# Optimization experiments

Measured on AMD Instinct MI355X. Metric: run time of the kernel, lower is better.

## Reference

```python
import jax, jax.numpy as jnp
import numpy as np
import math

F = 64        # num_features (multiplicity of each irrep)
N = 16000     # nodes
E = 256000    # edges (avg_num_neighbors = 16)
S = 4         # num_species
DE = 32       # scalar edge feature dim (radial basis)
W = 128       # interaction_mlp_width
AVG_NEIGH = 16.0
SQ2 = math.sqrt(2.0)
SQ3 = math.sqrt(3.0)


def setup_inputs() -> dict:
    key = jax.random.key(0)
    ks = jax.random.split(key, 32)
    def nrm(k, shape, scale=1.0):
        return jax.random.normal(k, shape, dtype=jnp.float32) * scale
    inp = {}
    # forward args
    inp["vectors"] = nrm(ks[0], (E, 1, 3))
    inp["lengths"] = jax.random.uniform(ks[1], (E, 1), dtype=jnp.float32)
    inp["node_s"] = nrm(ks[2], (N, F))            # 64x0e part of node_feats
    inp["node_v"] = nrm(ks[3], (N, F, 3))         # 64x1o part of node_feats
    inp["scalar_edge_feats"] = nrm(ks[4], (E, DE))
    inp["node_specie"] = jax.random.randint(ks[5], (N,), 0, S)
    inp["senders"] = jax.random.randint(ks[6], (E,), 0, N)
    inp["receivers"] = jax.random.randint(ks[7], (E,), 0, N)
    # parameters (e3nn Linear = per-irrep channel mixing, fan-in normalized; bias only on 0e)
    inp["W_up_s"] = nrm(ks[8], (F, F), F ** -0.5); inp["b_up_s"] = jnp.zeros((F,), jnp.float32)
    inp["W_up_v"] = nrm(ks[9], (F, F), F ** -0.5)
    din = 2 * F + DE + 1
    inp["mlp_W1"] = nrm(ks[10], (din, W), din ** -0.5); inp["mlp_b1"] = jnp.zeros((W,), jnp.float32)
    inp["mlp_W2"] = nrm(ks[11], (W, W), W ** -0.5); inp["mlp_b2"] = jnp.zeros((W,), jnp.float32)
    inp["mlp_W3"] = nrm(ks[12], (W, 3 * F), W ** -0.5); inp["mlp_b3"] = jnp.zeros((3 * F,), jnp.float32)
    inp["W_dn_s"] = nrm(ks[13], (F, F), F ** -0.5); inp["b_dn_s"] = jnp.zeros((F,), jnp.float32)
    inp["W_dn_v"] = nrm(ks[14], (2 * F, F), (2 * F) ** -0.5)
    # symmetric contraction weights (per species, per channel); correlation=2
    inp["w_sc_s"] = nrm(ks[15], (S, 3, F), 3 ** -0.5)   # paths to 0e: x0, x0^2, (x1.x1)/sqrt3
    inp["w_sc_v"] = nrm(ks[16], (S, 2, F), 2 ** -0.5)   # paths to 1o: x1, x0*x1
    inp["W_pb_s"] = nrm(ks[17], (F, F), F ** -0.5); inp["b_pb_s"] = jnp.zeros((F,), jnp.float32)
    inp["W_pb_v"] = nrm(ks[18], (F, F), F ** -0.5)
    inp["W_r1_s"] = nrm(ks[19], (F, 2 * F), F ** -0.5); inp["b_r1_s"] = jnp.zeros((2 * F,), jnp.float32)
    inp["W_r1_v"] = nrm(ks[20], (F, F), F ** -0.5)
    inp["W_r2_s"] = nrm(ks[21], (F, 1), F ** -0.5); inp["b_r2"] = jnp.zeros((1,), jnp.float32)
    inp["W_r2_v"] = nrm(ks[22], (F, 1), F ** -0.5)
    return inp


def reference(vectors, lengths, node_s, node_v, scalar_edge_feats, node_specie,
              senders, receivers,
              W_up_s, b_up_s, W_up_v,
              mlp_W1, mlp_b1, mlp_W2, mlp_b2, mlp_W3, mlp_b3,
              W_dn_s, b_dn_s, W_dn_v,
              w_sc_s, w_sc_v, W_pb_s, b_pb_s, W_pb_v,
              W_r1_s, b_r1_s, W_r1_v, W_r2_s, b_r2, W_r2_v):
    n = node_s.shape[0]
    # --- spherical harmonics, sh_irreps='1o', component normalization, normalize=False ---
    edge_v = SQ3 * vectors[:, 0, :]                              # [E,3]

    # --- InteractionBlock: linear_up ---
    h_s = node_s @ W_up_s + b_up_s                               # [N,F]
    h_v = jnp.einsum('nfi,fg->ngi', node_v, W_up_v)              # [N,F,3]

    # --- MessagePassingConvolution ---
    m_s = h_s[senders]                                           # [E,F] 0e
    m_v = h_v[senders]                                           # [E,F,3] 1o
    # tensor product with edge 1o, filtered to 0e+1o (unitary CG):
    tp_s = jnp.einsum('efi,ei->ef', m_v, edge_v) / SQ3           # 1o x 1o -> 0e  [E,F]
    tp_v1 = m_s[:, :, None] * edge_v[:, None, :]                 # 0e x 1o -> 1o  [E,F,3]
    tp_v2 = jnp.cross(m_v, edge_v[:, None, :]) / SQ2             # 1o x 1o -> 1o  [E,F,3]
    # scalar MLP mix (one scalar weight per output irrep = 3F)
    mlp_in = jnp.concatenate([m_s, h_s[receivers], scalar_edge_feats, lengths], axis=1)
    h = jax.nn.silu(mlp_in @ mlp_W1 + mlp_b1)
    h = jax.nn.silu(h @ mlp_W2 + mlp_b2)
    mix = h @ mlp_W3 + mlp_b3                                    # [E,3F]
    mix_s, mix_v1, mix_v2 = mix[:, :F], mix[:, F:2 * F], mix[:, 2 * F:]
    tp_s = tp_s * mix_s
    tp_v = jnp.concatenate([tp_v1 * mix_v1[:, :, None], tp_v2 * mix_v2[:, :, None]], axis=1)  # [E,2F,3]
    # scatter-add to receivers, normalize by avg_num_neighbors
    agg_s = jax.ops.segment_sum(tp_s, receivers, num_segments=n) / AVG_NEIGH   # [N,F]
    agg_v = jax.ops.segment_sum(tp_v, receivers, num_segments=n) / AVG_NEIGH   # [N,2F,3]
    # linear_down
    f_s = agg_s @ W_dn_s + b_dn_s                                # [N,F]
    f_v = jnp.einsum('nfi,fg->ngi', agg_v, W_dn_v)               # [N,F,3]

    # --- EquivariantProductBasisBlock: symmetric contraction (correlation=2), per-species ---
    ws = w_sc_s[node_specie]                                     # [N,3,F]
    wv = w_sc_v[node_specie]                                     # [N,2,F]
    vv = jnp.sum(f_v * f_v, axis=-1) / SQ3                       # 1o (x) 1o -> 0e, symmetric
    sc_s = ws[:, 0] * f_s + ws[:, 1] * (f_s * f_s) + ws[:, 2] * vv           # [N,F]
    sc_v = wv[:, 0][:, :, None] * f_v + wv[:, 1][:, :, None] * (f_s[:, :, None] * f_v)  # [N,F,3]
    p_s = sc_s @ W_pb_s + b_pb_s                                 # node_feats 0e out
    p_v = jnp.einsum('nfi,fg->ngi', sc_v, W_pb_v)                # node_feats 1o out

    # --- NonLinearReadoutBlock: linear to (2F x 0e + F x 1o), gate, linear to 1x0e+1x1o ---
    r_s = p_s @ W_r1_s + b_r1_s                                  # [N,2F]
    r_v = jnp.einsum('nfi,fg->ngi', p_v, W_r1_v)                 # [N,F,3]
    act = jax.nn.silu(r_s[:, :F])
    gates = jax.nn.silu(r_s[:, F:])
    g_v = gates[:, :, None] * r_v                                # gated vectors
    out_s = act @ W_r2_s + b_r2                                  # [N,1]  0e output
    out_v = jnp.einsum('nfi,fo->noi', g_v, W_r2_v)               # [N,1,3] 1o output
    return out_s, out_v, p_s, p_v
```

## Files before the change

kernel.cpp:

```cpp
#include <hip/hip_runtime.h>

typedef short bf16x8 __attribute__((ext_vector_type(8)));
typedef float f32x4  __attribute__((ext_vector_type(4)));
typedef unsigned short ushort_t;
typedef _Float16 half_t;

__device__ __forceinline__ float silu(float x) {
    float t = __expf(-x);
    return x * __builtin_amdgcn_rcpf(1.f + t);
}

__device__ __forceinline__ ushort_t f2bs(float x) {
    union { float f; unsigned int u; } v; v.f = x;
    unsigned int r = v.u + 0x7FFF + ((v.u >> 16) & 1);
    return (ushort_t)(r >> 16);
}
__device__ __forceinline__ ushort_t f2bs_t(float x) {
    union { float f; unsigned int u; } v; v.f = x;
    return (ushort_t)(v.u >> 16);
}
__device__ __forceinline__ float bs2f(ushort_t x) {
    union { unsigned int u; float f; } v; v.u = ((unsigned int)x) << 16; return v.f;
}

constexpr int N_   = 16000;
constexpr int E_   = 256000;
constexpr int Fd   = 64;

constexpr float SQ3f    = 1.7320508075688772f;
constexpr float INV_SQ3 = 0.5773502691896258f;
constexpr float INV_SQ2 = 0.7071067811865476f;
constexpr float INV_AVG = 0.0625f;

constexpr int OFF_OS = 0;
constexpr int OFF_OV = N_;
constexpr int OFF_PS = OFF_OV + 3 * N_;
constexpr int OFF_PV = OFF_PS + N_ * Fd;

constexpr int W1P_SZ = 6 * 8 * 512;
constexpr int W2P_SZ = 4 * 8 * 512;
constexpr int W3P_SZ = 4 * 12 * 512;

constexpr int CTR_W = 320;

__global__ __launch_bounds__(256) void pack_kernel(
    const float* __restrict__ W1, const float* __restrict__ W2,
    const float* __restrict__ W3,
    ushort_t* __restrict__ W1p, ushort_t* __restrict__ W2p,
    ushort_t* __restrict__ W3p)
{
    int idx = blockIdx.x * 256 + threadIdx.x;
    if (idx < W1P_SZ) {
        int j = idx & 7, lane = (idx >> 3) & 63, tile = idx >> 9;
        int c = tile >> 3, t = tile & 7;
        int k = c * 32 + (lane >> 4) * 8 + j;
        int n = t * 16 + (lane & 15);
        W1p[idx] = f2bs(k < 161 ? W1[k * 128 + n] : 0.f);
    } else if (idx < W1P_SZ + W2P_SZ) {
        int q = idx - W1P_SZ;
        int j = q & 7, lane = (q >> 3) & 63, tile = q >> 9;
        int c = tile >> 3, t = tile & 7;
        int k = c * 32 + (lane >> 4) * 8 + j;
        int n = t * 16 + (lane & 15);
        W2p[q] = f2bs(W2[k * 128 + n]);
    } else {
        int q = idx - W1P_SZ - W2P_SZ;
        int j = q & 7, lane = (q >> 3) & 63, tile = q >> 9;
        int c = tile / 12, t = tile % 12;
        int k = c * 32 + (lane >> 4) * 8 + j;
        int n = t * 16 + (lane & 15);
        W3p[q] = f2bs(W3[k * 192 + n]);
    }
}

__global__ __launch_bounds__(64, 4) void up_kernel(
    const float* __restrict__ node_s, const float* __restrict__ node_v,
    const float* __restrict__ W_up_s, const float* __restrict__ b_up_s,
    const float* __restrict__ W_up_v,
    const int* __restrict__ receivers, int* __restrict__ cnt,
    ushort_t* __restrict__ hs_bf, float* __restrict__ h_v)
{
    __shared__ float ns[4][64];
    __shared__ float nv[4][64][3];
    const int n0 = blockIdx.x * 4;
    const int g  = threadIdx.x;

    {
        int e = blockIdx.x * 64 + g;
        atomicAdd(&cnt[receivers[e]], 1);
    }

    #pragma unroll
    for (int j = 0; j < 4; j++) ns[j][g] = node_s[(n0 + j) * 64 + g];
    for (int idx = g; idx < 4 * 192; idx += 64) {
        int j = idx / 192, r = idx - j * 192;
        nv[j][r / 3][r % 3] = node_v[(size_t)n0 * 192 + idx];
    }
    __syncthreads();

    float as[4], a0[4], a1[4], a2[4];
    float bb = b_up_s[g];
    #pragma unroll
    for (int j = 0; j < 4; j++) { as[j] = bb; a0[j] = a1[j] = a2[j] = 0.f; }
    #pragma unroll 4
    for (int f = 0; f < 64; f++) {
        float wss = W_up_s[f * 64 + g];
        float wv  = W_up_v[f * 64 + g];
        #pragma unroll
        for (int j = 0; j < 4; j++) {
            as[j] += ns[j][f] * wss;
            a0[j] += nv[j][f][0] * wv;
            a1[j] += nv[j][f][1] * wv;
            a2[j] += nv[j][f][2] * wv;
        }
    }
    #pragma unroll
    for (int j = 0; j < 4; j++) {
        hs_bf[(n0 + j) * 64 + g] = f2bs(as[j]);
        h_v[(n0 + j) * 192 + 0 * 64 + g] = a0[j];
        h_v[(n0 + j) * 192 + 1 * 64 + g] = a1[j];
        h_v[(n0 + j) * 192 + 2 * 64 + g] = a2[j];
    }
}

__global__ __launch_bounds__(1024) void scan_kernel(
    const int* __restrict__ cnt, int* __restrict__ base, int* __restrict__ cursor)
{
    __shared__ int part[1024];
    const int t = threadIdx.x;
    int v[16];
    int s = 0;
    if (t < 1000) {
        const int4* c4 = (const int4*)(cnt + t * 16);
        #pragma unroll
        for (int q = 0; q < 4; q++) {
            int4 w = c4[q];
            v[q * 4 + 0] = w.x; v[q * 4 + 1] = w.y;
            v[q * 4 + 2] = w.z; v[q * 4 + 3] = w.w;
            s += w.x + w.y + w.z + w.w;
        }
    }
    part[t] = s;
    __syncthreads();
    for (int off = 1; off < 1024; off <<= 1) {
        int u = (t >= off) ? part[t - off] : 0;
        __syncthreads();
        part[t] += u;
        __syncthreads();
    }
    if (t < 1000) {
        int run = part[t] - s;
        int b[16];
        #pragma unroll
        for (int i = 0; i < 16; i++) { b[i] = run; run += v[i]; }
        int4* bb = (int4*)(base + t * 16);
        int4* cc = (int4*)(cursor + t * 16);
        #pragma unroll
        for (int q = 0; q < 4; q++) {
            int4 w = { b[q * 4], b[q * 4 + 1], b[q * 4 + 2], b[q * 4 + 3] };
            bb[q] = w;
            cc[q] = w;
        }
    }
}

__global__ __launch_bounds__(256, 3) void edge_mlp_kernel(
    const float* __restrict__ lengths, const float* __restrict__ sef,
    const int* __restrict__ senders, const int* __restrict__ receivers,
    const float* __restrict__ vectors,
    const float* __restrict__ b1f, const float* __restrict__ b2f,
    const float* __restrict__ b3f,
    const ushort_t* __restrict__ hs_bf, const float* __restrict__ h_v,
    const ushort_t* __restrict__ W1p, const ushort_t* __restrict__ W2p,
    const ushort_t* __restrict__ W3p,
    int* __restrict__ cursor, float4* __restrict__ evx,
    half_t* __restrict__ ctr)
{
    __shared__ ushort_t Als[64 * 200];
    __shared__ ushort_t Hs[64 * 136];
    __shared__ int perm_s[64];
    __shared__ int snd_s[64];
    __shared__ float ev_s[64][3];

    const int tid  = threadIdx.x;
    const int wave = tid >> 6, lane = tid & 63;
    const int quad = lane >> 4, l4 = lane & 15;
    const int e0   = blockIdx.x * 64;

    if (tid < 64) {
        int e = e0 + tid;
        int p = atomicAdd(&cursor[receivers[e]], 1);
        perm_s[tid] = p;
        snd_s[tid] = senders[e];
        float v0 = SQ3f * vectors[e * 3 + 0];
        float v1 = SQ3f * vectors[e * 3 + 1];
        float v2 = SQ3f * vectors[e * 3 + 2];
        ev_s[tid][0] = v0; ev_s[tid][1] = v1; ev_s[tid][2] = v2;
        float4 mt; mt.x = v0; mt.y = v1; mt.z = v2; mt.w = 0.f;
        evx[p] = mt;
    }

    {
        const int e  = tid & 63;
        const int ge = e0 + e;
        const int snd = senders[ge];
        const int rcv = receivers[ge];
        for (int c = tid >> 6; c < 24; c += 4) {
            bf16x8 v;
            if (c < 8) {
                v = *(const bf16x8*)(hs_bf + snd * 64 + c * 8);
            } else if (c < 16) {
                v = *(const bf16x8*)(hs_bf + rcv * 64 + (c - 8) * 8);
            } else if (c < 20) {
                const float4 s0 = *(const float4*)(sef + (size_t)ge * 32 + (c - 16) * 8);
                const float4 s1 = *(const float4*)(sef + (size_t)ge * 32 + (c - 16) * 8 + 4);
                v[0] = (short)f2bs(s0.x); v[1] = (short)f2bs(s0.y);
                v[2] = (short)f2bs(s0.z); v[3] = (short)f2bs(s0.w);
                v[4] = (short)f2bs(s1.x); v[5] = (short)f2bs(s1.y);
                v[6] = (short)f2bs(s1.z); v[7] = (short)f2bs(s1.w);
            } else if (c == 20) {
                v = (bf16x8){0,0,0,0,0,0,0,0};
                v[0] = (short)f2bs(lengths[ge]);
            } else {
                v = (bf16x8){0,0,0,0,0,0,0,0};
            }
            *(bf16x8*)(&Als[e * 200 + c * 8]) = v;
        }
    }
    __syncthreads();

    const bf16x8* B1 = (const bf16x8*)W1p;
    const bf16x8* B2 = (const bf16x8*)W2p;
    const bf16x8* B3 = (const bf16x8*)W3p;

    {
        f32x4 acc[2][4];
        #pragma unroll
        for (int ti = 0; ti < 2; ti++)
            #pragma unroll
            for (int m = 0; m < 4; m++) acc[ti][m] = (f32x4){0,0,0,0};
        #pragma unroll
        for (int c = 0; c < 6; c++) {
            bf16x8 b0 = B1[(c * 8 + wave * 2 + 0) * 64 + lane];
            bf16x8 b1 = B1[(c * 8 + wave * 2 + 1) * 64 + lane];
            #pragma unroll
            for (int m = 0; m < 4; m++) {
                bf16x8 a = *(const bf16x8*)(&Als[(m * 16 + l4) * 200 + c * 32 + quad * 8]);
                acc[0][m] = __builtin_amdgcn_mfma_f32_16x16x32_bf16(a, b0, acc[0][m], 0, 0, 0);
                acc[1][m] = __builtin_amdgcn_mfma_f32_16x16x32_bf16(a, b1, acc[1][m], 0, 0, 0);
            }
        }
        #pragma unroll
        for (int ti = 0; ti < 2; ti++) {
            int t = wave * 2 + ti;
            float bb = b1f[t * 16 + l4];
            #pragma unroll
            for (int m = 0; m < 4; m++)
                #pragma unroll
                for (int r = 0; r < 4; r++)
                    Hs[(m * 16 + quad * 4 + r) * 136 + t * 16 + l4] =
                        f2bs_t(silu(acc[ti][m][r] + bb));
        }
    }
    __syncthreads();

    {
        f32x4 acc[2][4];
        #pragma unroll
        for (int ti = 0; ti < 2; ti++)
            #pragma unroll
            for (int m = 0; m < 4; m++) acc[ti][m] = (f32x4){0,0,0,0};
        #pragma unroll
        for (int c = 0; c < 4; c++) {
            bf16x8 b0 = B2[(c * 8 + wave * 2 + 0) * 64 + lane];
            bf16x8 b1 = B2[(c * 8 + wave * 2 + 1) * 64 + lane];
            #pragma unroll
            for (int m = 0; m < 4; m++) {
                bf16x8 a = *(const bf16x8*)(&Hs[(m * 16 + l4) * 136 + c * 32 + quad * 8]);
                acc[0][m] = __builtin_amdgcn_mfma_f32_16x16x32_bf16(a, b0, acc[0][m], 0, 0, 0);
                acc[1][m] = __builtin_amdgcn_mfma_f32_16x16x32_bf16(a, b1, acc[1][m], 0, 0, 0);
            }
        }
        #pragma unroll
        for (int ti = 0; ti < 2; ti++) {
            int t = wave * 2 + ti;
            float bb = b2f[t * 16 + l4];
            #pragma unroll
            for (int m = 0; m < 4; m++)
                #pragma unroll
                for (int r = 0; r < 4; r++)
                    Als[(m * 16 + quad * 4 + r) * 136 + t * 16 + l4] =
                        f2bs_t(silu(acc[ti][m][r] + bb));
        }
    }
    __syncthreads();

    {
        f32x4 acc[3][4];
        #pragma unroll
        for (int ti = 0; ti < 3; ti++)
            #pragma unroll
            for (int m = 0; m < 4; m++) acc[ti][m] = (f32x4){0,0,0,0};
        #pragma unroll
        for (int c = 0; c < 4; c++) {
            bf16x8 b0 = B3[(c * 12 + wave * 3 + 0) * 64 + lane];
            bf16x8 b1 = B3[(c * 12 + wave * 3 + 1) * 64 + lane];
            bf16x8 b2 = B3[(c * 12 + wave * 3 + 2) * 64 + lane];
            #pragma unroll
            for (int m = 0; m < 4; m++) {
                bf16x8 a = *(const bf16x8*)(&Als[(m * 16 + l4) * 136 + c * 32 + quad * 8]);
                acc[0][m] = __builtin_amdgcn_mfma_f32_16x16x32_bf16(a, b0, acc[0][m], 0, 0, 0);
                acc[1][m] = __builtin_amdgcn_mfma_f32_16x16x32_bf16(a, b1, acc[1][m], 0, 0, 0);
                acc[2][m] = __builtin_amdgcn_mfma_f32_16x16x32_bf16(a, b2, acc[2][m], 0, 0, 0);
            }
        }
        __syncthreads();
        #pragma unroll
        for (int ti = 0; ti < 3; ti++) {
            int t = wave * 3 + ti;
            float bb = b3f[t * 16 + l4];
            #pragma unroll
            for (int m = 0; m < 4; m++)
                #pragma unroll
                for (int r = 0; r < 4; r++)
                    Als[(m * 16 + quad * 4 + r) * 200 + t * 16 + l4] =
                        f2bs(acc[ti][m][r] + bb);
        }
    }
    __syncthreads();

    {
        const int g = lane;
        #pragma unroll 4
        for (int j = 0; j < 16; j++) {
            const int el = wave * 16 + j;
            const int se = snd_s[el];
            const int p  = perm_s[el];
            const float ev0 = ev_s[el][0], ev1 = ev_s[el][1], ev2 = ev_s[el][2];
            const float m0 = h_v[(size_t)se * 192 + 0 * 64 + g];
            const float m1 = h_v[(size_t)se * 192 + 1 * 64 + g];
            const float m2 = h_v[(size_t)se * 192 + 2 * 64 + g];
            const float ms = bs2f(hs_bf[se * 64 + g]);
            const float mixs  = bs2f(Als[el * 200 +   0 + g]);
            const float mixv1 = bs2f(Als[el * 200 +  64 + g]);
            const float mixv2 = bs2f(Als[el * 200 + 128 + g]);
            half_t* row = ctr + (size_t)p * CTR_W;
            row[  0 + g] = (half_t)((m0 * ev0 + m1 * ev1 + m2 * ev2) * mixs);
            row[ 64 + g] = (half_t)(ms * mixv1);
            row[128 + g] = (half_t)((m1 * ev2 - m2 * ev1) * mixv2);
            row[192 + g] = (half_t)((m2 * ev0 - m0 * ev2) * mixv2);
            row[256 + g] = (half_t)((m0 * ev1 - m1 * ev0) * mixv2);
        }
    }
}

__global__ __launch_bounds__(256, 2) void node_fused_kernel(
    const int* __restrict__ base, const int* __restrict__ cnt,
    const float4* __restrict__ evx,
    const half_t* __restrict__ ctr,
    const int* __restrict__ specie,
    const float* __restrict__ W_dn_s, const float* __restrict__ b_dn_s,
    const float* __restrict__ W_dn_v,
    const float* __restrict__ w_sc_s, const float* __restrict__ w_sc_v,
    const float* __restrict__ W_pb_s, const float* __restrict__ b_pb_s,
    const float* __restrict__ W_pb_v,
    const float* __restrict__ W_r1_s, const float* __restrict__ b_r1_s,
    const float* __restrict__ W_r1_v,
    const float* __restrict__ W_r2_s, const float* __restrict__ b_r2,
    const float* __restrict__ W_r2_v,
    float* __restrict__ out)
{
    __shared__ float as_l[4][64];
    __shared__ float av_l[4][128][3];
    __shared__ float scs[4][64];
    __shared__ float scv[4][64][3];
    __shared__ float ps_[4][64];
    __shared__ float pv_[4][64][3];
    __shared__ float4 lmeta[4][64];

    const int tid = threadIdx.x;
    const int w   = tid >> 6;
    const int g   = tid & 63;
    const int n   = blockIdx.x * 4 + w;

    const int b = base[n];
    const int c = cnt[n];
    float accSa = 0.f, accSb = 0.f;
    float a10a = 0.f, a11a = 0.f, a12a = 0.f;
    float a20a = 0.f, a21a = 0.f, a22a = 0.f;
    float a10b = 0.f, a11b = 0.f, a12b = 0.f;
    float a20b = 0.f, a21b = 0.f, a22b = 0.f;

    for (int done = 0; done < c; done += 64) {
        int m = min(64, c - done);
        if (g < m) lmeta[w][g] = evx[b + done + g];
        int i = 0;
        for (; i + 1 < m; i += 2) {
            const float4 t1 = lmeta[w][i];
            const float4 t2 = lmeta[w][i + 1];
            const half_t* r1 = ctr + (size_t)(b + done + i) * CTR_W;
            const half_t* r2 = r1 + CTR_W;
            const float cs1 = (float)r1[g];
            const float k1  = (float)r1[64 + g];
            const float c10 = (float)r1[128 + g];
            const float c11 = (float)r1[192 + g];
            const float c12 = (float)r1[256 + g];
            const float cs2 = (float)r2[g];
            const float k2  = (float)r2[64 + g];
            const float c20 = (float)r2[128 + g];
            const float c21 = (float)r2[192 + g];
            const float c22 = (float)r2[256 + g];

            accSa += cs1; accSb += cs2;
            a10a += k1 * t1.x; a11a += k1 * t1.y; a12a += k1 * t1.z;
            a10b += k2 * t2.x; a11b += k2 * t2.y; a12b += k2 * t2.z;
            a20a += c10; a21a += c11; a22a += c12;
            a20b += c20; a21b += c21; a22b += c22;
        }
        if (i < m) {
            const float4 t1 = lmeta[w][i];
            const half_t* r1 = ctr + (size_t)(b + done + i) * CTR_W;
            const float cs1 = (float)r1[g];
            const float k1  = (float)r1[64 + g];
            accSa += cs1;
            a10a += k1 * t1.x; a11a += k1 * t1.y; a12a += k1 * t1.z;
            a20a += (float)r1[128 + g];
            a21a += (float)r1[192 + g];
            a22a += (float)r1[256 + g];
        }
    }
    as_l[w][g] = (accSa + accSb) * (INV_SQ3 * INV_AVG);
    av_l[w][g][0] = (a10a + a10b) * INV_AVG;
    av_l[w][g][1] = (a11a + a11b) * INV_AVG;
    av_l[w][g][2] = (a12a + a12b) * INV_AVG;
    av_l[w][64 + g][0] = (a20a + a20b) * (INV_SQ2 * INV_AVG);
    av_l[w][64 + g][1] = (a21a + a21b) * (INV_SQ2 * INV_AVG);
    av_l[w][64 + g][2] = (a22a + a22b) * (INV_SQ2 * INV_AVG);

    float f_s = b_dn_s[g];
    #pragma unroll 8
    for (int f = 0; f < 64; f++) f_s += as_l[w][f] * W_dn_s[f * 64 + g];
    float fv0 = 0.f, fv1 = 0.f, fv2 = 0.f;
    #pragma unroll 8
    for (int f = 0; f < 128; f++) {
        float wt = W_dn_v[f * 64 + g];
        fv0 += av_l[w][f][0] * wt;
        fv1 += av_l[w][f][1] * wt;
        fv2 += av_l[w][f][2] * wt;
    }

    float vv = (fv0 * fv0 + fv1 * fv1 + fv2 * fv2) * INV_SQ3;
    int sp = specie[n];
    float ws0 = w_sc_s[sp * 192 + 0 * 64 + g];
    float ws1 = w_sc_s[sp * 192 + 1 * 64 + g];
    float ws2 = w_sc_s[sp * 192 + 2 * 64 + g];
    float wv0 = w_sc_v[sp * 128 + 0 * 64 + g];
    float wv1 = w_sc_v[sp * 128 + 1 * 64 + g];
    float sc_s = ws0 * f_s + ws1 * f_s * f_s + ws2 * vv;
    float kv = wv0 + wv1 * f_s;
    scs[w][g] = sc_s;
    scv[w][g][0] = kv * fv0;
    scv[w][g][1] = kv * fv1;
    scv[w][g][2] = kv * fv2;

    float p_s = b_pb_s[g];
    float pv0 = 0.f, pv1 = 0.f, pv2 = 0.f;
    #pragma unroll 8
    for (int f = 0; f < 64; f++) {
        float wps = W_pb_s[f * 64 + g];
        p_s += scs[w][f] * wps;
        float wpv = W_pb_v[f * 64 + g];
        pv0 += scv[w][f][0] * wpv;
        pv1 += scv[w][f][1] * wpv;
        pv2 += scv[w][f][2] * wpv;
    }
    ps_[w][g] = p_s;
    pv_[w][g][0] = pv0; pv_[w][g][1] = pv1; pv_[w][g][2] = pv2;

    out[OFF_PS + n * 64 + g] = p_s;
    out[OFF_PV + (size_t)n * 192 + g * 3 + 0] = pv0;
    out[OFF_PV + (size_t)n * 192 + g * 3 + 1] = pv1;
    out[OFF_PV + (size_t)n * 192 + g * 3 + 2] = pv2;

    float r0 = b_r1_s[g];
    float r1 = b_r1_s[g + 64];
    float rv0 = 0.f, rv1 = 0.f, rv2 = 0.f;
    #pragma unroll 8
    for (int f = 0; f < 64; f++) {
        float p = ps_[w][f];
        r0 += p * W_r1_s[f * 128 + g];
        r1 += p * W_r1_s[f * 128 + g + 64];
        float wrv = W_r1_v[f * 64 + g];
        rv0 += pv_[w][f][0] * wrv;
        rv1 += pv_[w][f][1] * wrv;
        rv2 += pv_[w][f][2] * wrv;
    }
    float act  = silu(r0);
    float gate = silu(r1);
    float o_s = act * W_r2_s[g];
    float wr2v = W_r2_v[g];
    float ov0 = gate * rv0 * wr2v;
    float ov1 = gate * rv1 * wr2v;
    float ov2 = gate * rv2 * wr2v;

    #pragma unroll
    for (int off = 32; off > 0; off >>= 1) {
        o_s += __shfl_down(o_s, off);
        ov0 += __shfl_down(ov0, off);
        ov1 += __shfl_down(ov1, off);
        ov2 += __shfl_down(ov2, off);
    }
    if (g == 0) {
        out[OFF_OS + n] = o_s + b_r2[0];
        out[OFF_OV + n * 3 + 0] = ov0;
        out[OFF_OV + n * 3 + 1] = ov1;
        out[OFF_OV + n * 3 + 2] = ov2;
    }
}

extern "C" void kernel_launch(void* const* d_in, const int* in_sizes, int n_in,
                              void* d_out, int out_size, void* d_ws, size_t ws_size,
                              hipStream_t stream)
{
    const float* vectors  = (const float*)d_in[0];
    const float* lengths  = (const float*)d_in[1];
    const float* node_s   = (const float*)d_in[2];
    const float* node_v   = (const float*)d_in[3];
    const float* sef      = (const float*)d_in[4];
    const int*  specie    = (const int*)d_in[5];
    const int*  senders   = (const int*)d_in[6];
    const int*  receivers = (const int*)d_in[7];
    const float* W_up_s   = (const float*)d_in[8];
    const float* b_up_s   = (const float*)d_in[9];
    const float* W_up_v   = (const float*)d_in[10];
    const float* mlp_W1   = (const float*)d_in[11];
    const float* mlp_b1   = (const float*)d_in[12];
    const float* mlp_W2   = (const float*)d_in[13];
    const float* mlp_b2   = (const float*)d_in[14];
    const float* mlp_W3   = (const float*)d_in[15];
    const float* mlp_b3   = (const float*)d_in[16];
    const float* W_dn_s   = (const float*)d_in[17];
    const float* b_dn_s   = (const float*)d_in[18];
    const float* W_dn_v   = (const float*)d_in[19];
    const float* w_sc_s   = (const float*)d_in[20];
    const float* w_sc_v   = (const float*)d_in[21];
    const float* W_pb_s   = (const float*)d_in[22];
    const float* b_pb_s   = (const float*)d_in[23];
    const float* W_pb_v   = (const float*)d_in[24];
    const float* W_r1_s   = (const float*)d_in[25];
    const float* b_r1_s   = (const float*)d_in[26];
    const float* W_r1_v   = (const float*)d_in[27];
    const float* W_r2_s   = (const float*)d_in[28];
    const float* b_r2     = (const float*)d_in[29];
    const float* W_r2_v   = (const float*)d_in[30];

    float* h_v = (float*)d_ws;
    half_t* ctr = (half_t*)(h_v + (size_t)N_ * 192);
    ushort_t* hs_bf = (ushort_t*)(ctr + (size_t)E_ * CTR_W);
    ushort_t* W1p   = hs_bf + (size_t)N_ * 64;
    ushort_t* W2p   = W1p + W1P_SZ;
    ushort_t* W3p   = W2p + W2P_SZ;
    float4* evx     = (float4*)((((size_t)(W3p + W3P_SZ)) + 15) & ~(size_t)15);
    int* cnt        = (int*)(evx + E_);
    int* base       = cnt + N_;
    int* cursor     = base + N_;

    float* out = (float*)d_out;

    hipMemsetAsync(cnt, 0, N_ * sizeof(int), stream);

    up_kernel<<<N_ / 4, 64, 0, stream>>>(node_s, node_v, W_up_s, b_up_s, W_up_v,
                                         receivers, cnt, hs_bf, h_v);
    pack_kernel<<<256, 256, 0, stream>>>(mlp_W1, mlp_W2, mlp_W3, W1p, W2p, W3p);
    scan_kernel<<<1, 1024, 0, stream>>>(cnt, base, cursor);

    edge_mlp_kernel<<<E_ / 64, 256, 0, stream>>>(
        lengths, sef, senders, receivers, vectors,
        mlp_b1, mlp_b2, mlp_b3,
        hs_bf, h_v, W1p, W2p, W3p, cursor, evx, ctr);

    node_fused_kernel<<<N_ / 4, 256, 0, stream>>>(
        base, cnt, evx,
        ctr, specie,
        W_dn_s, b_dn_s, W_dn_v, w_sc_s, w_sc_v,
        W_pb_s, b_pb_s, W_pb_v, W_r1_s, b_r1_s, W_r1_v,
        W_r2_s, b_r2, W_r2_v, out);
}
```

Before: 389.0 us.

## Process edges in receiver-sorted order and segment-reduce with atomics instead of staging

```diff
diff --git a/kernel.cpp b/kernel.cpp
--- a/kernel.cpp
+++ b/kernel.cpp
@@ -3,7 +3,6 @@
 typedef short bf16x8 __attribute__((ext_vector_type(8)));
 typedef float f32x4  __attribute__((ext_vector_type(4)));
 typedef unsigned short ushort_t;
-typedef _Float16 half_t;
 
 __device__ __forceinline__ float silu(float x) {
     float t = __expf(-x);
@@ -41,7 +40,7 @@
 constexpr int W2P_SZ = 4 * 8 * 512;
 constexpr int W3P_SZ = 4 * 12 * 512;
 
-constexpr int CTR_W = 320;
+constexpr int AGG_W = 448;
 
 __global__ __launch_bounds__(256) void pack_kernel(
     const float* __restrict__ W1, const float* __restrict__ W2,
@@ -164,22 +163,31 @@
     }
 }
 
+__global__ __launch_bounds__(256) void perm_kernel(
+    const int* __restrict__ receivers, int* __restrict__ cursor,
+    int* __restrict__ eid)
+{
+    int e = blockIdx.x * 256 + threadIdx.x;
+    int r = receivers[e];
+    int p = atomicAdd(&cursor[r], 1);
+    eid[p] = e;
+}
+
 __global__ __launch_bounds__(256, 3) void edge_mlp_kernel(
     const float* __restrict__ lengths, const float* __restrict__ sef,
     const int* __restrict__ senders, const int* __restrict__ receivers,
-    const float* __restrict__ vectors,
+    const float* __restrict__ vectors, const int* __restrict__ eid,
     const float* __restrict__ b1f, const float* __restrict__ b2f,
     const float* __restrict__ b3f,
     const ushort_t* __restrict__ hs_bf, const float* __restrict__ h_v,
     const ushort_t* __restrict__ W1p, const ushort_t* __restrict__ W2p,
     const ushort_t* __restrict__ W3p,
-    int* __restrict__ cursor, float4* __restrict__ evx,
-    half_t* __restrict__ ctr)
+    float* __restrict__ agg)
 {
     __shared__ ushort_t Als[64 * 200];
     __shared__ ushort_t Hs[64 * 136];
-    __shared__ int perm_s[64];
     __shared__ int snd_s[64];
+    __shared__ int rcv_s[64];
     __shared__ float ev_s[64][3];
 
     const int tid  = threadIdx.x;
@@ -188,21 +196,17 @@
     const int e0   = blockIdx.x * 64;
 
     if (tid < 64) {
-        int e = e0 + tid;
-        int p = atomicAdd(&cursor[receivers[e]], 1);
-        perm_s[tid] = p;
+        int e = eid[e0 + tid];
         snd_s[tid] = senders[e];
-        float v0 = SQ3f * vectors[e * 3 + 0];
-        float v1 = SQ3f * vectors[e * 3 + 1];
-        float v2 = SQ3f * vectors[e * 3 + 2];
-        ev_s[tid][0] = v0; ev_s[tid][1] = v1; ev_s[tid][2] = v2;
-        float4 mt; mt.x = v0; mt.y = v1; mt.z = v2; mt.w = 0.f;
-        evx[p] = mt;
+        rcv_s[tid] = receivers[e];
+        ev_s[tid][0] = SQ3f * vectors[e * 3 + 0];
+        ev_s[tid][1] = SQ3f * vectors[e * 3 + 1];
+        ev_s[tid][2] = SQ3f * vectors[e * 3 + 2];
     }
 
     {
         const int e  = tid & 63;
-        const int ge = e0 + e;
+        const int ge = eid[e0 + e];
         const int snd = senders[ge];
         const int rcv = receivers[ge];
         for (int c = tid >> 6; c < 24; c += 4) {
@@ -330,34 +334,59 @@
     __syncthreads();
 
     {
-        const int g = lane;
-        #pragma unroll 4
-        for (int j = 0; j < 16; j++) {
-            const int el = wave * 16 + j;
-            const int se = snd_s[el];
-            const int p  = perm_s[el];
-            const float ev0 = ev_s[el][0], ev1 = ev_s[el][1], ev2 = ev_s[el][2];
-            const float m0 = h_v[(size_t)se * 192 + 0 * 64 + g];
-            const float m1 = h_v[(size_t)se * 192 + 1 * 64 + g];
-            const float m2 = h_v[(size_t)se * 192 + 2 * 64 + g];
-            const float ms = bs2f(hs_bf[se * 64 + g]);
-            const float mixs  = bs2f(Als[el * 200 +   0 + g]);
-            const float mixv1 = bs2f(Als[el * 200 +  64 + g]);
-            const float mixv2 = bs2f(Als[el * 200 + 128 + g]);
-            half_t* row = ctr + (size_t)p * CTR_W;
-            row[  0 + g] = (half_t)((m0 * ev0 + m1 * ev1 + m2 * ev2) * mixs);
-            row[ 64 + g] = (half_t)(ms * mixv1);
-            row[128 + g] = (half_t)((m1 * ev2 - m2 * ev1) * mixv2);
-            row[192 + g] = (half_t)((m2 * ev0 - m0 * ev2) * mixv2);
-            row[256 + g] = (half_t)((m0 * ev1 - m1 * ev0) * mixv2);
-        }
+        const int g  = lane;
+        const int p0 = wave * 16;
+        float acc0 = 0.f, acc1 = 0.f, acc2 = 0.f, acc3 = 0.f;
+        float acc4 = 0.f, acc5 = 0.f, acc6 = 0.f;
+        int cur = rcv_s[p0];
+
+        for (int jj = 0; jj < 16; jj += 8) {
+            float M0[8], M1[8], M2[8], MS[8];
+            #pragma unroll
+            for (int j = 0; j < 8; j++) {
+                const int se = snd_s[p0 + jj + j];
+                M0[j] = h_v[(size_t)se * 192 + 0 * 64 + g];
+                M1[j] = h_v[(size_t)se * 192 + 1 * 64 + g];
+                M2[j] = h_v[(size_t)se * 192 + 2 * 64 + g];
+                MS[j] = bs2f(hs_bf[se * 64 + g]);
+            }
+            #pragma unroll
+            for (int j = 0; j < 8; j++) {
+                const int el = p0 + jj + j;
+                const int r  = rcv_s[el];
+                if (r != cur) {
+                    float* a = agg + (size_t)cur * AGG_W + g;
+                    atomicAdd(a +   0, acc0); atomicAdd(a +  64, acc1);
+                    atomicAdd(a + 128, acc2); atomicAdd(a + 192, acc3);
+                    atomicAdd(a + 256, acc4); atomicAdd(a + 320, acc5);
+                    atomicAdd(a + 384, acc6);
+                    acc0 = acc1 = acc2 = acc3 = acc4 = acc5 = acc6 = 0.f;
+                    cur = r;
+                }
+                const float ev0 = ev_s[el][0], ev1 = ev_s[el][1], ev2 = ev_s[el][2];
+                const float mixs  = bs2f(Als[el * 200 +   0 + g]);
+                const float mixv1 = bs2f(Als[el * 200 +  64 + g]);
+                const float mixv2 = bs2f(Als[el * 200 + 128 + g]);
+                const float k = MS[j] * mixv1;
+                acc0 += (M0[j] * ev0 + M1[j] * ev1 + M2[j] * ev2) * mixs;
+                acc1 += k * ev0;
+                acc2 += k * ev1;
+                acc3 += k * ev2;
+                acc4 += (M1[j] * ev2 - M2[j] * ev1) * mixv2;
+                acc5 += (M2[j] * ev0 - M0[j] * ev2) * mixv2;
+                acc6 += (M0[j] * ev1 - M1[j] * ev0) * mixv2;
+            }
+        }
+        float* a = agg + (size_t)cur * AGG_W + g;
+        atomicAdd(a +   0, acc0); atomicAdd(a +  64, acc1);
+        atomicAdd(a + 128, acc2); atomicAdd(a + 192, acc3);
+        atomicAdd(a + 256, acc4); atomicAdd(a + 320, acc5);
+        atomicAdd(a + 384, acc6);
     }
 }
 
 __global__ __launch_bounds__(256, 2) void node_fused_kernel(
-    const int* __restrict__ base, const int* __restrict__ cnt,
-    const float4* __restrict__ evx,
-    const half_t* __restrict__ ctr,
+    const float* __restrict__ agg,
     const int* __restrict__ specie,
     const float* __restrict__ W_dn_s, const float* __restrict__ b_dn_s,
     const float* __restrict__ W_dn_v,
@@ -376,66 +405,20 @@
     __shared__ float scv[4][64][3];
     __shared__ float ps_[4][64];
     __shared__ float pv_[4][64][3];
-    __shared__ float4 lmeta[4][64];
 
     const int tid = threadIdx.x;
     const int w   = tid >> 6;
     const int g   = tid & 63;
     const int n   = blockIdx.x * 4 + w;
 
-    const int b = base[n];
-    const int c = cnt[n];
-    float accSa = 0.f, accSb = 0.f;
-    float a10a = 0.f, a11a = 0.f, a12a = 0.f;
-    float a20a = 0.f, a21a = 0.f, a22a = 0.f;
-    float a10b = 0.f, a11b = 0.f, a12b = 0.f;
-    float a20b = 0.f, a21b = 0.f, a22b = 0.f;
-
-    for (int done = 0; done < c; done += 64) {
-        int m = min(64, c - done);
-        if (g < m) lmeta[w][g] = evx[b + done + g];
-        int i = 0;
-        for (; i + 1 < m; i += 2) {
-            const float4 t1 = lmeta[w][i];
-            const float4 t2 = lmeta[w][i + 1];
-            const half_t* r1 = ctr + (size_t)(b + done + i) * CTR_W;
-            const half_t* r2 = r1 + CTR_W;
-            const float cs1 = (float)r1[g];
-            const float k1  = (float)r1[64 + g];
-            const float c10 = (float)r1[128 + g];
-            const float c11 = (float)r1[192 + g];
-            const float c12 = (float)r1[256 + g];
-            const float cs2 = (float)r2[g];
-            const float k2  = (float)r2[64 + g];
-            const float c20 = (float)r2[128 + g];
-            const float c21 = (float)r2[192 + g];
-            const float c22 = (float)r2[256 + g];
-
-            accSa += cs1; accSb += cs2;
-            a10a += k1 * t1.x; a11a += k1 * t1.y; a12a += k1 * t1.z;
-            a10b += k2 * t2.x; a11b += k2 * t2.y; a12b += k2 * t2.z;
-            a20a += c10; a21a += c11; a22a += c12;
-            a20b += c20; a21b += c21; a22b += c22;
-        }
-        if (i < m) {
-            const float4 t1 = lmeta[w][i];
-            const half_t* r1 = ctr + (size_t)(b + done + i) * CTR_W;
-            const float cs1 = (float)r1[g];
-            const float k1  = (float)r1[64 + g];
-            accSa += cs1;
-            a10a += k1 * t1.x; a11a += k1 * t1.y; a12a += k1 * t1.z;
-            a20a += (float)r1[128 + g];
-            a21a += (float)r1[192 + g];
-            a22a += (float)r1[256 + g];
-        }
-    }
-    as_l[w][g] = (accSa + accSb) * (INV_SQ3 * INV_AVG);
-    av_l[w][g][0] = (a10a + a10b) * INV_AVG;
-    av_l[w][g][1] = (a11a + a11b) * INV_AVG;
-    av_l[w][g][2] = (a12a + a12b) * INV_AVG;
-    av_l[w][64 + g][0] = (a20a + a20b) * (INV_SQ2 * INV_AVG);
-    av_l[w][64 + g][1] = (a21a + a21b) * (INV_SQ2 * INV_AVG);
-    av_l[w][64 + g][2] = (a22a + a22b) * (INV_SQ2 * INV_AVG);
+    const float* ag = agg + (size_t)n * AGG_W;
+    as_l[w][g]        = ag[g]       * (INV_SQ3 * INV_AVG);
+    av_l[w][g][0]     = ag[ 64 + g] * INV_AVG;
+    av_l[w][g][1]     = ag[128 + g] * INV_AVG;
+    av_l[w][g][2]     = ag[192 + g] * INV_AVG;
+    av_l[w][64 + g][0] = ag[256 + g] * (INV_SQ2 * INV_AVG);
+    av_l[w][64 + g][1] = ag[320 + g] * (INV_SQ2 * INV_AVG);
+    av_l[w][64 + g][2] = ag[384 + g] * (INV_SQ2 * INV_AVG);
 
     float f_s = b_dn_s[g];
     #pragma unroll 8
@@ -554,34 +537,35 @@
     const float* b_r2     = (const float*)d_in[29];
     const float* W_r2_v   = (const float*)d_in[30];
 
-    float* h_v = (float*)d_ws;
-    half_t* ctr = (half_t*)(h_v + (size_t)N_ * 192);
-    ushort_t* hs_bf = (ushort_t*)(ctr + (size_t)E_ * CTR_W);
+    float* h_v   = (float*)d_ws;
+    float* agg   = h_v + (size_t)N_ * 192;
+    ushort_t* hs_bf = (ushort_t*)(agg + (size_t)N_ * AGG_W);
     ushort_t* W1p   = hs_bf + (size_t)N_ * 64;
     ushort_t* W2p   = W1p + W1P_SZ;
     ushort_t* W3p   = W2p + W2P_SZ;
-    float4* evx     = (float4*)((((size_t)(W3p + W3P_SZ)) + 15) & ~(size_t)15);
-    int* cnt        = (int*)(evx + E_);
+    int* eid        = (int*)((((size_t)(W3p + W3P_SZ)) + 15) & ~(size_t)15);
+    int* cnt        = eid + E_;
     int* base       = cnt + N_;
     int* cursor     = base + N_;
 
     float* out = (float*)d_out;
 
     hipMemsetAsync(cnt, 0, N_ * sizeof(int), stream);
+    hipMemsetAsync(agg, 0, (size_t)N_ * AGG_W * sizeof(float), stream);
 
     up_kernel<<<N_ / 4, 64, 0, stream>>>(node_s, node_v, W_up_s, b_up_s, W_up_v,
                                          receivers, cnt, hs_bf, h_v);
     pack_kernel<<<256, 256, 0, stream>>>(mlp_W1, mlp_W2, mlp_W3, W1p, W2p, W3p);
     scan_kernel<<<1, 1024, 0, stream>>>(cnt, base, cursor);
+    perm_kernel<<<E_ / 256, 256, 0, stream>>>(receivers, cursor, eid);
 
     edge_mlp_kernel<<<E_ / 64, 256, 0, stream>>>(
-        lengths, sef, senders, receivers, vectors,
+        lengths, sef, senders, receivers, vectors, eid,
         mlp_b1, mlp_b2, mlp_b3,
-        hs_bf, h_v, W1p, W2p, W3p, cursor, evx, ctr);
+        hs_bf, h_v, W1p, W2p, W3p, agg);
 
     node_fused_kernel<<<N_ / 4, 256, 0, stream>>>(
-        base, cnt, evx,
-        ctr, specie,
+        agg, specie,
         W_dn_s, b_dn_s, W_dn_v, w_sc_s, w_sc_v,
         W_pb_s, b_pb_s, W_pb_v, W_r1_s, b_r1_s, W_r1_v,
         W_r2_s, b_r2, W_r2_v, out);
```

After: 374.1 us. 1.04x faster.
